# Kernel tuning notes

Hardware: AMD Instinct MI355X
Metric: run time of the kernel (lower is better)

Reference implementation:

```python
import jax, jax.numpy as jnp
import numpy as np

N_NODES = 100000
N_EDGES = 1600000
HIDDEN = 128
VOCAB = 2048


def setup_inputs() -> dict:
    key = jax.random.key(0)
    k1, k2, k3, k4 = jax.random.split(key, 4)
    x = jax.random.normal(k1, (N_NODES, HIDDEN), dtype=jnp.float32)
    edge_index = jax.random.randint(k2, (2, N_EDGES), 0, N_NODES, dtype=jnp.int64)
    # torch Linear default init ~ U(-1/sqrt(fan_in), 1/sqrt(fan_in)); scale randn similarly
    W_trn = jax.random.normal(k3, (HIDDEN, HIDDEN), dtype=jnp.float32) / np.sqrt(HIDDEN)
    b_trn = jnp.zeros((HIDDEN,), dtype=jnp.float32)
    W_prd = jax.random.normal(k4, (HIDDEN, VOCAB), dtype=jnp.float32) / np.sqrt(HIDDEN)
    b_prd = jnp.zeros((VOCAB,), dtype=jnp.float32)
    return {"x": x, "edge_index": edge_index, "W_trn": W_trn, "b_trn": b_trn,
            "W_prd": W_prd, "b_prd": b_prd}


def reference(x, edge_index, W_trn, b_trn, W_prd, b_prd):
    # GINConv(nn=Identity, eps=0): out[i] = x[i] + sum_{j -> i} x[j]
    src = edge_index[0]  # message sources
    dst = edge_index[1]  # aggregation targets
    agg = jax.ops.segment_sum(x[src], dst, num_segments=x.shape[0])  # [N, H]
    h = x + agg
    h = h @ W_trn + b_trn          # [N, H]
    logits = h @ W_prd + b_prd     # [N, vocab]
    return logits
```

## Files before the change

### kernel.cpp

```cpp
#include <hip/hip_runtime.h>
#include <hip/hip_bf16.h>

#define HIDDEN 128
#define VOCAB  2048
#define CAP    64

using frag_ab = __attribute__((ext_vector_type(8))) short;
using frag_cd = __attribute__((ext_vector_type(4))) float;

static __device__ __forceinline__ unsigned short f2bf(float f) {
    __hip_bfloat16 b = __float2bfloat16(f);
    return *reinterpret_cast<unsigned short*>(&b);
}
static __device__ __forceinline__ float bflo(unsigned int w) {
    return __uint_as_float(w << 16);
}
static __device__ __forceinline__ float bfhi(unsigned int w) {
    return __uint_as_float(w & 0xffff0000u);
}

__global__ void prep_kernel(const float* __restrict__ Wt,
                            const float* __restrict__ Wp,
                            const float* __restrict__ bt,
                            const float* __restrict__ bp,
                            const float4* __restrict__ x4,
                            unsigned short* __restrict__ wfT,
                            float* __restrict__ bfv,
                            int* __restrict__ deg,
                            uint2* __restrict__ xb4,
                            int M, int gM)
{
    int b = blockIdx.x;
    int tid = threadIdx.x;
    if (b < 1024) {
        int gid = b * 256 + tid;
        int n = gid & 2047;
        int k = gid >> 11;
        float acc = 0.f;
#pragma unroll 8
        for (int j = 0; j < 128; ++j)
            acc += Wt[k * 128 + j] * Wp[j * 2048 + n];
        wfT[n * 128 + k] = f2bf(acc);
    } else if (b < 1032) {
        int n = (b - 1024) * 256 + tid;
        float acc = bp[n];
#pragma unroll 8
        for (int j = 0; j < 128; ++j)
            acc += bt[j] * Wp[j * 2048 + n];
        bfv[n] = acc;
    } else if (b < 1032 + gM) {
        int i = (b - 1032) * 256 + tid;
        if (i < M) deg[i] = 0;
    } else {
        int i = (b - 1032 - gM) * 256 + tid;
        int n4 = M * 32;
        if (i < n4) {
            float4 v = x4[i];
            uint2 o;
            o.x = (unsigned int)f2bf(v.x) | ((unsigned int)f2bf(v.y) << 16);
            o.y = (unsigned int)f2bf(v.z) | ((unsigned int)f2bf(v.w) << 16);
            xb4[i] = o;
        }
    }
}

__global__ void bucket_fill_kernel(const int* __restrict__ ei,
                                   int* __restrict__ deg,
                                   int* __restrict__ srclist, int n_edges)
{
    int e = blockIdx.x * 256 + threadIdx.x;
    if (e < n_edges) {
        int d = ei[n_edges + e];
        int pos = atomicAdd(&deg[d], 1);
        if (pos < CAP)
            srclist[(size_t)d * CAP + pos] = ei[e];
    }
}

__global__ void gather_kernel(const uint2* __restrict__ xb4,
                              const int* __restrict__ deg,
                              const int* __restrict__ srclist,
                              uint2* __restrict__ hb4, int n)
{
    int t = blockIdx.x * 256 + threadIdx.x;
    int pair = t >> 6;
    int lane = t & 63;
    int half = lane >> 5;
    int hl   = lane & 31;
    int node = pair * 2 + half;
    if (node >= n) return;

    uint2 self = xb4[(size_t)node * 32 + hl];
    float a0 = bflo(self.x), a1 = bfhi(self.x);
    float a2 = bflo(self.y), a3 = bfhi(self.y);

    int len = deg[node];
    if (len > CAP) len = CAP;
    size_t base = (size_t)node * CAP;

    int cl = hl < len ? hl : (len > 0 ? len - 1 : 0);
    int eidx = srclist[base + cl];

    for (int e = 0; e < len; e += 8) {
        if (e == 32) {
            int cl2 = 32 + hl < len ? 32 + hl : len - 1;
            eidx = srclist[base + cl2];
        }
        uint2 w[8];
#pragma unroll
        for (int j = 0; j < 8; ++j) {
            int ee = e + j; if (ee >= len) ee = len - 1;
            int idx = __shfl(eidx, (half << 5) | (ee & 31));
            w[j] = xb4[(size_t)idx * 32 + hl];
        }
#pragma unroll
        for (int j = 0; j < 8; ++j) {
            if (e + j < len) {
                a0 += bflo(w[j].x); a1 += bfhi(w[j].x);
                a2 += bflo(w[j].y); a3 += bfhi(w[j].y);
            }
        }
    }
    uint2 o;
    o.x = (unsigned int)f2bf(a0) | ((unsigned int)f2bf(a1) << 16);
    o.y = (unsigned int)f2bf(a2) | ((unsigned int)f2bf(a3) << 16);
    hb4[(size_t)node * 32 + hl] = o;
}

__global__ __launch_bounds__(256, 2) void gemm_kernel(
    const unsigned short* __restrict__ hbf,
    const unsigned short* __restrict__ wfT,
    const float* __restrict__ bfv,
    float* __restrict__ out, int M)
{
    int tid  = threadIdx.x;
    int wave = tid >> 6;
    int lane = tid & 63;
    int wm = wave >> 1, wn = wave & 1;
    int brow   = blockIdx.y * 128;
    int cbase0 = blockIdx.x * 512;

    int lr = lane & 15;
    int lk = (lane >> 4) * 8;
    int lq = lk >> 3;

    frag_ab a[4][4];
#pragma unroll
    for (int mi = 0; mi < 4; ++mi) {
        int r = brow + wm * 64 + mi * 16 + lr;
        if (r > M - 1) r = M - 1;
        const frag_ab* p = reinterpret_cast<const frag_ab*>(&hbf[(size_t)r * HIDDEN]);
#pragma unroll
        for (int kk = 0; kk < 4; ++kk)
            a[mi][kk] = p[kk * 4 + lq];
    }

#pragma unroll
    for (int c = 0; c < 4; ++c) {
        int cb = cbase0 + c * 128 + wn * 64;
        frag_cd acc[4][4] = {};
#pragma unroll
        for (int kk = 0; kk < 4; ++kk) {
            frag_ab b[4];
#pragma unroll
            for (int ni = 0; ni < 4; ++ni) {
                int nr = cb + ni * 16 + lr;
                b[ni] = *reinterpret_cast<const frag_ab*>(
                    &wfT[(size_t)nr * HIDDEN + kk * 32 + lk]);
            }
#pragma unroll
            for (int mi = 0; mi < 4; ++mi)
#pragma unroll
                for (int ni = 0; ni < 4; ++ni)
                    acc[mi][ni] = __builtin_amdgcn_mfma_f32_16x16x32_bf16(
                        b[ni], a[mi][kk], acc[mi][ni], 0, 0, 0);
        }

        int nq = (lane >> 4) * 4;
#pragma unroll
        for (int mi = 0; mi < 4; ++mi) {
            int grow = brow + wm * 64 + mi * 16 + lr;
            if (grow >= M) continue;
            size_t ro = (size_t)grow * VOCAB;
#pragma unroll
            for (int ni = 0; ni < 4; ++ni) {
                int gcol = cb + ni * 16 + nq;
                float4 b4 = *reinterpret_cast<const float4*>(&bfv[gcol]);
                float4 o;
                o.x = acc[mi][ni][0] + b4.x;
                o.y = acc[mi][ni][1] + b4.y;
                o.z = acc[mi][ni][2] + b4.z;
                o.w = acc[mi][ni][3] + b4.w;
                *reinterpret_cast<float4*>(&out[ro + gcol]) = o;
            }
        }
    }
}

extern "C" void kernel_launch(void* const* d_in, const int* in_sizes, int n_in,
                              void* d_out, int out_size, void* d_ws, size_t ws_size,
                              hipStream_t stream) {
    const float* x  = (const float*)d_in[0];
    const int*   ei = (const int*)d_in[1];
    const float* Wt = (const float*)d_in[2];
    const float* bt = (const float*)d_in[3];
    const float* Wp = (const float*)d_in[4];
    const float* bp = (const float*)d_in[5];
    float* out = (float*)d_out;

    int M       = in_sizes[0] / HIDDEN;
    int n_edges = in_sizes[1] / 2;

    char* ws = (char*)d_ws;
    size_t off = 0;
    auto alloc = [&](size_t bytes) { char* p = ws + off; off += (bytes + 15) & ~(size_t)15; return p; };
    unsigned short* wfT     = (unsigned short*)alloc((size_t)VOCAB * HIDDEN * 2);
    float*          bfv     = (float*)alloc(VOCAB * 4);
    int*            deg     = (int*)alloc((size_t)M * 4);
    int*            srclist = (int*)alloc((size_t)M * CAP * 4);
    unsigned short* hb      = (unsigned short*)alloc((size_t)M * HIDDEN * 2);
    unsigned short* xb      = (unsigned short*)alloc((size_t)M * HIDDEN * 2);

    int gM = (M + 255) / 256;
    int gC = (M * 32 + 255) / 256;
    prep_kernel<<<1032 + gM + gC, 256, 0, stream>>>(Wt, Wp, bt, bp, (const float4*)x,
                                                    wfT, bfv, deg, (uint2*)xb, M, gM);

    int gE = (n_edges + 255) / 256;
    bucket_fill_kernel<<<gE, 256, 0, stream>>>(ei, deg, srclist, n_edges);

    int gG = (M * 32 + 255) / 256;
    gather_kernel<<<gG, 256, 0, stream>>>((const uint2*)xb, deg, srclist,
                                          (uint2*)hb, M);

    dim3 grid(VOCAB / 512, (M + 127) / 128);
    gemm_kernel<<<grid, 256, 0, stream>>>(hb, wfT, bfv, out, M);
}
```

Baseline: 429.5 us.

## Fuse all stages into one cooperative persistent kernel with grid syncs

Replaces the four separate launches (prep, bucket fill, gather, GEMM) with a single cooperative kernel of 512 blocks that runs each stage as a grid-stride loop, separated by grid-wide barriers. The GEMM becomes a persistent loop over 128x128 output tiles, where before each block covered 128 rows by 512 columns. The goal is to remove launch gaps and tail effects between stages. The cost is grid.sync overhead and a fixed 512-block grid, which may under-occupy the gather and GEMM phases and reloads A fragments once per column tile. The old multi-kernel path is kept as a fallback if the cooperative launch fails.

```diff
diff --git a/kernel.cpp b/kernel.cpp
--- a/kernel.cpp
+++ b/kernel.cpp
@@ -1,5 +1,8 @@
 #include <hip/hip_runtime.h>
 #include <hip/hip_bf16.h>
+#include <hip/hip_cooperative_groups.h>
+
+namespace cg = cooperative_groups;
 
 #define HIDDEN 128
 #define VOCAB  2048
@@ -17,6 +20,182 @@
 }
 static __device__ __forceinline__ float bfhi(unsigned int w) {
     return __uint_as_float(w & 0xffff0000u);
+}
+
+__global__ __launch_bounds__(256, 2) void mega_kernel(
+    const float* __restrict__ x, const int* __restrict__ ei,
+    const float* __restrict__ Wt, const float* __restrict__ bt,
+    const float* __restrict__ Wp, const float* __restrict__ bp,
+    unsigned short* __restrict__ wfT, float* __restrict__ bfv,
+    int* __restrict__ deg, int* __restrict__ srclist,
+    unsigned short* __restrict__ xb, unsigned short* __restrict__ hb,
+    float* __restrict__ out, int M, int n_edges)
+{
+    cg::grid_group grid = cg::this_grid();
+    int tid  = threadIdx.x;
+    int gtid = blockIdx.x * 256 + tid;
+    int nthr = gridDim.x * 256;
+
+    for (int i = gtid; i < M; i += nthr) deg[i] = 0;
+    for (int n = gtid; n < VOCAB; n += nthr) {
+        float acc = bp[n];
+#pragma unroll 8
+        for (int j = 0; j < 128; ++j)
+            acc += bt[j] * Wp[j * 2048 + n];
+        bfv[n] = acc;
+    }
+    grid.sync();
+
+    for (int e = gtid; e < n_edges; e += nthr) {
+        int d = ei[n_edges + e];
+        int pos = atomicAdd(&deg[d], 1);
+        if (pos < CAP)
+            srclist[(size_t)d * CAP + pos] = ei[e];
+    }
+    for (int g = gtid; g < VOCAB * HIDDEN; g += nthr) {
+        int n = g & 2047;
+        int k = g >> 11;
+        float acc = 0.f;
+#pragma unroll 8
+        for (int j = 0; j < 128; ++j)
+            acc += Wt[k * 128 + j] * Wp[j * 2048 + n];
+        wfT[n * 128 + k] = f2bf(acc);
+    }
+    {
+        const float4* x4 = reinterpret_cast<const float4*>(x);
+        uint2* xb4 = reinterpret_cast<uint2*>(xb);
+        int n4 = M * 32;
+        for (int i = gtid; i < n4; i += nthr) {
+            float4 v = x4[i];
+            uint2 o;
+            o.x = (unsigned int)f2bf(v.x) | ((unsigned int)f2bf(v.y) << 16);
+            o.y = (unsigned int)f2bf(v.z) | ((unsigned int)f2bf(v.w) << 16);
+            xb4[i] = o;
+        }
+    }
+    grid.sync();
+
+    {
+        const uint2* xb4 = reinterpret_cast<const uint2*>(xb);
+        uint2* hb4 = reinterpret_cast<uint2*>(hb);
+        int wid   = blockIdx.x * 4 + (tid >> 6);
+        int nwave = gridDim.x * 4;
+        int lane  = tid & 63;
+        int half  = lane >> 5;
+        int hl    = lane & 31;
+        int npair = (M + 1) >> 1;
+        for (int p = wid; p < npair; p += nwave) {
+            int node  = p * 2 + half;
+            bool alive = node < M;
+            float a0 = 0.f, a1 = 0.f, a2 = 0.f, a3 = 0.f;
+            int len = 0;
+            size_t base = 0;
+            int eidx = 0;
+            if (alive) {
+                uint2 self = xb4[(size_t)node * 32 + hl];
+                a0 = bflo(self.x); a1 = bfhi(self.x);
+                a2 = bflo(self.y); a3 = bfhi(self.y);
+                len = deg[node];
+                if (len > CAP) len = CAP;
+                base = (size_t)node * CAP;
+                int cl = hl < len ? hl : (len > 0 ? len - 1 : 0);
+                eidx = srclist[base + cl];
+            }
+            for (int e = 0; e < len; e += 8) {
+                if (e == 32) {
+                    int cl2 = 32 + hl < len ? 32 + hl : len - 1;
+                    eidx = srclist[base + cl2];
+                }
+                uint2 w[8];
+#pragma unroll
+                for (int j = 0; j < 8; ++j) {
+                    int ee = e + j; if (ee >= len) ee = len - 1;
+                    int idx = __shfl(eidx, (half << 5) | (ee & 31));
+                    w[j] = xb4[(size_t)idx * 32 + hl];
+                }
+#pragma unroll
+                for (int j = 0; j < 8; ++j) {
+                    if (e + j < len) {
+                        a0 += bflo(w[j].x); a1 += bfhi(w[j].x);
+                        a2 += bflo(w[j].y); a3 += bfhi(w[j].y);
+                    }
+                }
+            }
+            if (alive) {
+                uint2 o;
+                o.x = (unsigned int)f2bf(a0) | ((unsigned int)f2bf(a1) << 16);
+                o.y = (unsigned int)f2bf(a2) | ((unsigned int)f2bf(a3) << 16);
+                hb4[(size_t)node * 32 + hl] = o;
+            }
+        }
+    }
+    grid.sync();
+
+    {
+        int wave = tid >> 6;
+        int lane = tid & 63;
+        int wm = wave >> 1, wn = wave & 1;
+        int lr = lane & 15;
+        int lk = (lane >> 4) * 8;
+        int lq = lk >> 3;
+        int nq = (lane >> 4) * 4;
+
+        int ntile = (M + 127) >> 7;
+        int ntask = ntile * 16;
+        for (int task = blockIdx.x; task < ntask; task += gridDim.x) {
+            int c    = task & 15;
+            int by   = task >> 4;
+            int brow = by * 128;
+            int cb   = c * 128 + wn * 64;
+
+            frag_ab a[4][4];
+#pragma unroll
+            for (int mi = 0; mi < 4; ++mi) {
+                int r = brow + wm * 64 + mi * 16 + lr;
+                if (r > M - 1) r = M - 1;
+                const frag_ab* p = reinterpret_cast<const frag_ab*>(&hb[(size_t)r * HIDDEN]);
+#pragma unroll
+                for (int kk = 0; kk < 4; ++kk)
+                    a[mi][kk] = p[kk * 4 + lq];
+            }
+
+            frag_cd acc[4][4] = {};
+#pragma unroll
+            for (int kk = 0; kk < 4; ++kk) {
+                frag_ab b[4];
+#pragma unroll
+                for (int ni = 0; ni < 4; ++ni) {
+                    int nr = cb + ni * 16 + lr;
+                    b[ni] = *reinterpret_cast<const frag_ab*>(
+                        &wfT[(size_t)nr * HIDDEN + kk * 32 + lk]);
+                }
+#pragma unroll
+                for (int mi = 0; mi < 4; ++mi)
+#pragma unroll
+                    for (int ni = 0; ni < 4; ++ni)
+                        acc[mi][ni] = __builtin_amdgcn_mfma_f32_16x16x32_bf16(
+                            b[ni], a[mi][kk], acc[mi][ni], 0, 0, 0);
+            }
+#pragma unroll
+            for (int mi = 0; mi < 4; ++mi) {
+                int grow = brow + wm * 64 + mi * 16 + lr;
+                if (grow < M) {
+                    size_t ro = (size_t)grow * VOCAB;
+#pragma unroll
+                    for (int ni = 0; ni < 4; ++ni) {
+                        int gcol = cb + ni * 16 + nq;
+                        float4 b4 = *reinterpret_cast<const float4*>(&bfv[gcol]);
+                        float4 o;
+                        o.x = acc[mi][ni][0] + b4.x;
+                        o.y = acc[mi][ni][1] + b4.y;
+                        o.z = acc[mi][ni][2] + b4.z;
+                        o.w = acc[mi][ni][3] + b4.w;
+                        *reinterpret_cast<float4*>(&out[ro + gcol]) = o;
+                    }
+                }
+            }
+        }
+    }
 }
 
 __global__ void prep_kernel(const float* __restrict__ Wt,
@@ -221,18 +400,25 @@
     unsigned short* hb      = (unsigned short*)alloc((size_t)M * HIDDEN * 2);
     unsigned short* xb      = (unsigned short*)alloc((size_t)M * HIDDEN * 2);
 
-    int gM = (M + 255) / 256;
-    int gC = (M * 32 + 255) / 256;
-    prep_kernel<<<1032 + gM + gC, 256, 0, stream>>>(Wt, Wp, bt, bp, (const float4*)x,
-                                                    wfT, bfv, deg, (uint2*)xb, M, gM);
-
-    int gE = (n_edges + 255) / 256;
-    bucket_fill_kernel<<<gE, 256, 0, stream>>>(ei, deg, srclist, n_edges);
-
-    int gG = (M * 32 + 255) / 256;
-    gather_kernel<<<gG, 256, 0, stream>>>((const uint2*)xb, deg, srclist,
-                                          (uint2*)hb, M);
-
-    dim3 grid(VOCAB / 512, (M + 127) / 128);
-    gemm_kernel<<<grid, 256, 0, stream>>>(hb, wfT, bfv, out, M);
-}
+    void* args[] = {(void*)&x, (void*)&ei, (void*)&Wt, (void*)&bt, (void*)&Wp,
+                    (void*)&bp, (void*)&wfT, (void*)&bfv, (void*)&deg,
+                    (void*)&srclist, (void*)&xb, (void*)&hb, (void*)&out,
+                    (void*)&M, (void*)&n_edges};
+    hipError_t err = hipLaunchCooperativeKernel((const void*)mega_kernel,
+                                                dim3(512), dim3(256),
+                                                args, 0, stream);
+    if (err != hipSuccess) {
+        (void)hipGetLastError();
+        int gM = (M + 255) / 256;
+        int gC = (M * 32 + 255) / 256;
+        prep_kernel<<<1032 + gM + gC, 256, 0, stream>>>(Wt, Wp, bt, bp, (const float4*)x,
+                                                        wfT, bfv, deg, (uint2*)xb, M, gM);
+        int gE = (n_edges + 255) / 256;
+        bucket_fill_kernel<<<gE, 256, 0, stream>>>(ei, deg, srclist, n_edges);
+        int gG = (M * 32 + 255) / 256;
+        gather_kernel<<<gG, 256, 0, stream>>>((const uint2*)xb, deg, srclist,
+                                              (uint2*)hb, M);
+        dim3 grid(VOCAB / 512, (M + 127) / 128);
+        gemm_kernel<<<grid, 256, 0, stream>>>(hb, wfT, bfv, out, M);
+    }
+}
```

Measured after the change: 716.0 us. +66.7%, slower.

## Fuse neighbor gather into GEMM via shared-memory tile of aggregated rows

Applied to the files above, without the earlier changes.

Merges the gather and GEMM kernels. Each block aggregates 32 nodes into a padded LDS tile, then runs MFMA against all 2048 output columns. This removes the hb intermediate write and re-read and one launch. In exchange, blocks cover only 32 rows, so each block streams the whole wfT (512KB), relying on L2 and lowering MFMA reuse per B load. The latency-bound gather phase and the MFMA phase are now serialized within each block.

```diff
diff --git a/kernel.cpp b/kernel.cpp
--- a/kernel.cpp
+++ b/kernel.cpp
@@ -4,6 +4,7 @@
 #define HIDDEN 128
 #define VOCAB  2048
 #define CAP    64
+#define LDT    136
 
 using frag_ab = __attribute__((ext_vector_type(8))) short;
 using frag_cd = __attribute__((ext_vector_type(4))) float;
@@ -77,88 +78,81 @@
     }
 }
 
-__global__ void gather_kernel(const uint2* __restrict__ xb4,
-                              const int* __restrict__ deg,
-                              const int* __restrict__ srclist,
-                              uint2* __restrict__ hb4, int n)
-{
-    int t = blockIdx.x * 256 + threadIdx.x;
-    int pair = t >> 6;
-    int lane = t & 63;
-    int half = lane >> 5;
-    int hl   = lane & 31;
-    int node = pair * 2 + half;
-    if (node >= n) return;
-
-    uint2 self = xb4[(size_t)node * 32 + hl];
-    float a0 = bflo(self.x), a1 = bfhi(self.x);
-    float a2 = bflo(self.y), a3 = bfhi(self.y);
-
-    int len = deg[node];
-    if (len > CAP) len = CAP;
-    size_t base = (size_t)node * CAP;
-
-    int cl = hl < len ? hl : (len > 0 ? len - 1 : 0);
-    int eidx = srclist[base + cl];
-
-    for (int e = 0; e < len; e += 8) {
-        if (e == 32) {
-            int cl2 = 32 + hl < len ? 32 + hl : len - 1;
-            eidx = srclist[base + cl2];
-        }
-        uint2 w[8];
-#pragma unroll
-        for (int j = 0; j < 8; ++j) {
-            int ee = e + j; if (ee >= len) ee = len - 1;
-            int idx = __shfl(eidx, (half << 5) | (ee & 31));
-            w[j] = xb4[(size_t)idx * 32 + hl];
-        }
-#pragma unroll
-        for (int j = 0; j < 8; ++j) {
-            if (e + j < len) {
-                a0 += bflo(w[j].x); a1 += bfhi(w[j].x);
-                a2 += bflo(w[j].y); a3 += bfhi(w[j].y);
-            }
-        }
-    }
-    uint2 o;
-    o.x = (unsigned int)f2bf(a0) | ((unsigned int)f2bf(a1) << 16);
-    o.y = (unsigned int)f2bf(a2) | ((unsigned int)f2bf(a3) << 16);
-    hb4[(size_t)node * 32 + hl] = o;
-}
-
-__global__ __launch_bounds__(256, 2) void gemm_kernel(
-    const unsigned short* __restrict__ hbf,
+__global__ __launch_bounds__(256, 4) void gg_kernel(
+    const uint2* __restrict__ xb4,
+    const int* __restrict__ deg,
+    const int* __restrict__ srclist,
     const unsigned short* __restrict__ wfT,
     const float* __restrict__ bfv,
     float* __restrict__ out, int M)
 {
+    __shared__ unsigned short hs[32 * LDT];
+
     int tid  = threadIdx.x;
     int wave = tid >> 6;
     int lane = tid & 63;
-    int wm = wave >> 1, wn = wave & 1;
-    int brow   = blockIdx.y * 128;
-    int cbase0 = blockIdx.x * 512;
+    int half = lane >> 5;
+    int hl   = lane & 31;
+    int brow = blockIdx.x * 32;
+
+    for (int p = 0; p < 4; ++p) {
+        int nd   = wave * 8 + p * 2 + half;
+        int node = brow + nd;
+        bool alive = node < M;
+        float a0 = 0.f, a1 = 0.f, a2 = 0.f, a3 = 0.f;
+        int len = 0; size_t base = 0; int eidx = 0;
+        if (alive) {
+            uint2 self = xb4[(size_t)node * 32 + hl];
+            a0 = bflo(self.x); a1 = bfhi(self.x);
+            a2 = bflo(self.y); a3 = bfhi(self.y);
+            len = deg[node];
+            if (len > CAP) len = CAP;
+            base = (size_t)node * CAP;
+            int cl = hl < len ? hl : (len > 0 ? len - 1 : 0);
+            eidx = srclist[base + cl];
+        }
+        for (int e = 0; e < len; e += 8) {
+            if (e == 32) {
+                int cl2 = 32 + hl < len ? 32 + hl : len - 1;
+                eidx = srclist[base + cl2];
+            }
+            uint2 w[8];
+#pragma unroll
+            for (int j = 0; j < 8; ++j) {
+                int ee = e + j; if (ee >= len) ee = len - 1;
+                int idx = __shfl(eidx, (half << 5) | (ee & 31));
+                w[j] = xb4[(size_t)idx * 32 + hl];
+            }
+#pragma unroll
+            for (int j = 0; j < 8; ++j) {
+                if (e + j < len) {
+                    a0 += bflo(w[j].x); a1 += bfhi(w[j].x);
+                    a2 += bflo(w[j].y); a3 += bfhi(w[j].y);
+                }
+            }
+        }
+        uint2 o;
+        o.x = (unsigned int)f2bf(a0) | ((unsigned int)f2bf(a1) << 16);
+        o.y = (unsigned int)f2bf(a2) | ((unsigned int)f2bf(a3) << 16);
+        *reinterpret_cast<uint2*>(&hs[nd * LDT + hl * 4]) = o;
+    }
+    __syncthreads();
 
     int lr = lane & 15;
     int lk = (lane >> 4) * 8;
-    int lq = lk >> 3;
-
-    frag_ab a[4][4];
-#pragma unroll
-    for (int mi = 0; mi < 4; ++mi) {
-        int r = brow + wm * 64 + mi * 16 + lr;
-        if (r > M - 1) r = M - 1;
-        const frag_ab* p = reinterpret_cast<const frag_ab*>(&hbf[(size_t)r * HIDDEN]);
+    int nq = (lane >> 4) * 4;
+
+    frag_ab a[2][4];
+#pragma unroll
+    for (int mi = 0; mi < 2; ++mi)
 #pragma unroll
         for (int kk = 0; kk < 4; ++kk)
-            a[mi][kk] = p[kk * 4 + lq];
-    }
-
-#pragma unroll
-    for (int c = 0; c < 4; ++c) {
-        int cb = cbase0 + c * 128 + wn * 64;
-        frag_cd acc[4][4] = {};
+            a[mi][kk] = *reinterpret_cast<const frag_ab*>(
+                &hs[(mi * 16 + lr) * LDT + kk * 32 + lk]);
+
+    for (int c = 0; c < 8; ++c) {
+        int cb = wave * 512 + c * 64;
+        frag_cd acc[2][4] = {};
 #pragma unroll
         for (int kk = 0; kk < 4; ++kk) {
             frag_ab b[4];
@@ -169,29 +163,28 @@
                     &wfT[(size_t)nr * HIDDEN + kk * 32 + lk]);
             }
 #pragma unroll
-            for (int mi = 0; mi < 4; ++mi)
+            for (int mi = 0; mi < 2; ++mi)
 #pragma unroll
                 for (int ni = 0; ni < 4; ++ni)
                     acc[mi][ni] = __builtin_amdgcn_mfma_f32_16x16x32_bf16(
                         b[ni], a[mi][kk], acc[mi][ni], 0, 0, 0);
         }
-
-        int nq = (lane >> 4) * 4;
-#pragma unroll
-        for (int mi = 0; mi < 4; ++mi) {
-            int grow = brow + wm * 64 + mi * 16 + lr;
-            if (grow >= M) continue;
-            size_t ro = (size_t)grow * VOCAB;
-#pragma unroll
-            for (int ni = 0; ni < 4; ++ni) {
-                int gcol = cb + ni * 16 + nq;
-                float4 b4 = *reinterpret_cast<const float4*>(&bfv[gcol]);
-                float4 o;
-                o.x = acc[mi][ni][0] + b4.x;
-                o.y = acc[mi][ni][1] + b4.y;
-                o.z = acc[mi][ni][2] + b4.z;
-                o.w = acc[mi][ni][3] + b4.w;
-                *reinterpret_cast<float4*>(&out[ro + gcol]) = o;
+#pragma unroll
+        for (int mi = 0; mi < 2; ++mi) {
+            int grow = brow + mi * 16 + lr;
+            if (grow < M) {
+                size_t ro = (size_t)grow * VOCAB;
+#pragma unroll
+                for (int ni = 0; ni < 4; ++ni) {
+                    int gcol = cb + ni * 16 + nq;
+                    float4 b4 = *reinterpret_cast<const float4*>(&bfv[gcol]);
+                    float4 o;
+                    o.x = acc[mi][ni][0] + b4.x;
+                    o.y = acc[mi][ni][1] + b4.y;
+                    o.z = acc[mi][ni][2] + b4.z;
+                    o.w = acc[mi][ni][3] + b4.w;
+                    *reinterpret_cast<float4*>(&out[ro + gcol]) = o;
+                }
             }
         }
     }
@@ -218,7 +211,6 @@
     float*          bfv     = (float*)alloc(VOCAB * 4);
     int*            deg     = (int*)alloc((size_t)M * 4);
     int*            srclist = (int*)alloc((size_t)M * CAP * 4);
-    unsigned short* hb      = (unsigned short*)alloc((size_t)M * HIDDEN * 2);
     unsigned short* xb      = (unsigned short*)alloc((size_t)M * HIDDEN * 2);
 
     int gM = (M + 255) / 256;
@@ -229,10 +221,7 @@
     int gE = (n_edges + 255) / 256;
     bucket_fill_kernel<<<gE, 256, 0, stream>>>(ei, deg, srclist, n_edges);
 
-    int gG = (M * 32 + 255) / 256;
-    gather_kernel<<<gG, 256, 0, stream>>>((const uint2*)xb, deg, srclist,
-                                          (uint2*)hb, M);
-
-    dim3 grid(VOCAB / 512, (M + 127) / 128);
-    gemm_kernel<<<grid, 256, 0, stream>>>(hb, wfT, bfv, out, M);
-}
+    int gG = (M + 31) / 32;
+    gg_kernel<<<gG, 256, 0, stream>>>((const uint2*)xb, deg, srclist,
+                                      wfT, bfv, out, M);
+}
```

Measured after the change: 485.7 us. 1.13x slower.
